# Performance work log

Measured on AMD Instinct MI355X. Metric: run time of the kernel, lower is better.

The kernel has to match this reference:

```python
import jax, jax.numpy as jnp
import numpy as np

DIM = 128
L = 4
EPS = 1e-5


def setup_inputs() -> dict:
    key = jax.random.key(0)
    ks = jax.random.split(key, 16)
    g, n_per = 4096, 32
    n = g * n_per
    e = 4 * n
    s = 0.05
    inp = {
        "x_atoms": jax.random.randint(ks[0], (n, 2), 0, 3),
        "edge_index": jax.random.randint(ks[1], (2, e), 0, n),
        "edge_attr": jax.random.randint(ks[2], (e, 2), 0, 3),
        "batch": jnp.repeat(jnp.arange(g), n_per),
        "num_graphs": g,
        "max_nodes": n_per,
        "task_embs": jax.random.normal(ks[3], (g, DIM), jnp.float32),
        "teb": jax.random.normal(ks[4], (g, DIM), jnp.float32),
        "emb1": jax.random.normal(ks[5], (120, DIM), jnp.float32) * s,
        "emb2": jax.random.normal(ks[6], (3, DIM), jnp.float32) * s,
        "edge_e1": jax.random.normal(ks[7], (L, 6, DIM), jnp.float32) * s,
        "edge_e2": jax.random.normal(ks[8], (L, 3, DIM), jnp.float32) * s,
        "W1": jax.random.normal(ks[9], (L, DIM, 2 * DIM), jnp.float32) * s,
        "b1": jnp.zeros((L, 2 * DIM), jnp.float32),
        "W2": jax.random.normal(ks[10], (L, 2 * DIM, DIM), jnp.float32) * s,
        "b2": jnp.zeros((L, DIM), jnp.float32),
        "bn_w": jnp.ones((L, DIM), jnp.float32),
        "bn_b": jnp.zeros((L, DIM), jnp.float32),
        "film_Wg": jax.random.normal(ks[11], (2, DIM, DIM), jnp.float32) * s,
        "film_bg": jnp.zeros((2, DIM), jnp.float32),
        "film_Wb": jax.random.normal(ks[12], (2, DIM, DIM), jnp.float32) * s,
        "film_bb": jnp.zeros((2, DIM), jnp.float32),
    }
    return inp


def _gin_layer(x, src, dst, eattr, e1, e2, W1, b1, W2, b2):
    # GINConv (pretrain-gnns): scatter-add of (x_j + edge_emb) + self-loop (attr [4,0]), then 2-layer MLP.
    n = x.shape[0]
    emb = e1[eattr[:, 0]] + e2[eattr[:, 1]]                       # [E, D]
    agg = jax.ops.segment_sum(x[src] + emb, dst, num_segments=n)  # [N, D]
    agg = agg + x + (e1[4] + e2[0])                               # self loops
    h = jax.nn.relu(agg @ W1 + b1)
    return h @ W2 + b2


def _batchnorm(x, w, b):
    mu = jnp.mean(x, axis=0)
    var = jnp.var(x, axis=0)
    return (x - mu) * jax.lax.rsqrt(var + EPS) * w + b


def reference(x_atoms, edge_index, edge_attr, batch, num_graphs, max_nodes,
              task_embs, teb, emb1, emb2, edge_e1, edge_e2,
              W1, b1, W2, b2, bn_w, bn_b,
              film_Wg, film_bg, film_Wb, film_bb):
    g = int(num_graphs)
    n = x_atoms.shape[0]
    x = emb1[x_atoms[:, 0]] + emb2[x_atoms[:, 1]]                 # [N, D]
    # --- add virtual nodes (one per graph) and bidirectional virtual edges ---
    x = jnp.concatenate([x, teb], axis=0)                         # [N+g, D]
    dst0 = jnp.arange(n)
    vsrc = n + batch                                              # virtual node index per real node
    src_all = jnp.concatenate([edge_index[0], vsrc, dst0])
    dst_all = jnp.concatenate([edge_index[1], dst0, vsrc])
    v_attr = jnp.tile(jnp.array([[5, 0]], dtype=edge_attr.dtype), (2 * n, 1))
    eattr = jnp.concatenate([edge_attr, v_attr], axis=0)
    # --- positions within graph for to_dense_batch (batch is sorted) ---
    counts = jnp.bincount(batch, length=g)
    offsets = jnp.cumsum(counts) - counts
    pos = dst0 - offsets[batch]
    for layer in range(L):
        x = _gin_layer(x, src_all, dst_all, eattr,
                       edge_e1[layer], edge_e2[layer],
                       W1[layer], b1[layer], W2[layer], b2[layer])
        if layer in (1, 3):
            xv = x[n:]
            dense = jnp.zeros((g, int(max_nodes), DIM), x.dtype).at[batch, pos].set(x[:n])
            fl = layer // 3
            gamma = task_embs @ film_Wg[fl] + film_bg[fl]          # [g, D]
            beta = task_embs @ film_Wb[fl] + film_bb[fl]
            dense = gamma[:, None, :] * dense + beta[:, None, :]
            x = jnp.concatenate([dense[batch, pos], xv], axis=0)   # masked_select inverse
        x = _batchnorm(x, bn_w[layer], bn_b[layer])
        if layer != L - 1:
            x = jax.nn.relu(x)
        # dropout is identity in eval mode
    return x[:n]
```

## Files before the change

kernel.cpp:

```cpp
#include <hip/hip_runtime.h>
#include <hip/hip_bf16.h>

typedef __bf16 bf16_t;
typedef bf16_t bf16x8 __attribute__((ext_vector_type(8)));
typedef bf16_t bf16x4v __attribute__((ext_vector_type(4)));
typedef float f32x4 __attribute__((ext_vector_type(4)));

#define EPSV 1e-5f

__global__ void k_zerof(float* p, int cnt) {
  int i = blockIdx.x * 256 + threadIdx.x;
  if (i < cnt) p[i] = 0.f;
}
__global__ void k_zeroi(int* p, int cnt) {
  int i = blockIdx.x * 256 + threadIdx.x;
  if (i < cnt) p[i] = 0;
}

__global__ void k_prep_weights(const float* __restrict__ W1, const float* __restrict__ W2,
                               bf16_t* __restrict__ W1T, bf16_t* __restrict__ W2T, int total) {
  int idx = blockIdx.x * 256 + threadIdx.x;
  if (idx >= total) return;
  int l = idx >> 15, r = idx & 32767;
  int k = r >> 8, c = r & 255;
  W1T[(l << 15) + c * 128 + k] = (bf16_t)W1[idx];
  int k2 = r >> 7, c2 = r & 127;
  W2T[(l << 15) + c2 * 256 + k2] = (bf16_t)W2[idx];
}

__global__ void k_prep_film(const float* __restrict__ Wg, const float* __restrict__ Wb,
                            bf16_t* __restrict__ fWT) {
  int idx = blockIdx.x * 256 + threadIdx.x;
  if (idx >= 4 * 16384) return;
  int m = idx >> 14, r = idx & 16383;
  int c = r >> 7, k = r & 127;
  const float* W = ((m & 1) ? Wb : Wg) + (m >> 1) * 16384;
  fWT[idx] = (bf16_t)W[k * 128 + c];
}

__global__ void k_prep_te(const float* __restrict__ te, bf16_t* __restrict__ teb_out, int total) {
  int idx = blockIdx.x * 256 + threadIdx.x;
  if (idx < total) teb_out[idx] = (bf16_t)te[idx];
}

__global__ void k_ecomb(const float* __restrict__ e1, const float* __restrict__ e2,
                        float* __restrict__ ec, int total) {
  int idx = blockIdx.x * 256 + threadIdx.x;
  if (idx >= total) return;
  int ch = idx & 127;
  int t = idx >> 7;
  int comb = t % 18, l = t / 18;
  int i = comb / 3, j = comb % 3;
  ec[idx] = e1[(l * 6 + i) * 128 + ch] + e2[(l * 3 + j) * 128 + ch];
}

__launch_bounds__(256, 2)
__global__ void k_film(const bf16_t* __restrict__ teb, const bf16_t* __restrict__ fWT,
                       const float* __restrict__ bg, const float* __restrict__ bb,
                       float* __restrict__ gbuf, int g) {
  const int mat = blockIdx.x & 3;
  const int r0 = (blockIdx.x >> 2) * 64;
  const int tid = threadIdx.x;
  const int wave = tid >> 6, lane = tid & 63;
  const int lr = lane & 15, lk = lane >> 4;
  const int w32 = wave * 32;
  const bf16_t* W = fWT + mat * 16384;
  const float* B = ((mat & 1) ? bb : bg) + (mat >> 1) * 128;

  bf16x8 bbf[2][4];
  #pragma unroll
  for (int cf = 0; cf < 2; ++cf)
    #pragma unroll
    for (int kk = 0; kk < 4; ++kk)
      bbf[cf][kk] = *(const bf16x8*)(W + ((w32 + cf * 16 + lr) << 7) + kk * 32 + (lk << 3));

  f32x4 acc[4][2];
  f32x4 zero4 = {0.f, 0.f, 0.f, 0.f};
  #pragma unroll
  for (int rf = 0; rf < 4; ++rf)
    #pragma unroll
    for (int cf = 0; cf < 2; ++cf) acc[rf][cf] = zero4;

  #pragma unroll
  for (int kk = 0; kk < 4; ++kk) {
    bf16x8 a[4];
    #pragma unroll
    for (int rf = 0; rf < 4; ++rf)
      a[rf] = *(const bf16x8*)(teb + ((size_t)(r0 + rf * 16 + lr) << 7) + kk * 32 + (lk << 3));
    #pragma unroll
    for (int rf = 0; rf < 4; ++rf)
      #pragma unroll
      for (int cf = 0; cf < 2; ++cf)
        acc[rf][cf] = __builtin_amdgcn_mfma_f32_16x16x32_bf16(a[rf], bbf[cf][kk], acc[rf][cf], 0, 0, 0);
  }

  float* out = gbuf + (size_t)mat * g * 128;
  #pragma unroll
  for (int cf = 0; cf < 2; ++cf) {
    int col = w32 + cf * 16 + lr;
    float bias = B[col];
    #pragma unroll
    for (int rf = 0; rf < 4; ++rf)
      #pragma unroll
      for (int j = 0; j < 4; ++j) {
        int row = r0 + rf * 16 + lk * 4 + j;
        out[(size_t)row * 128 + col] = acc[rf][cf][j] + bias;
      }
  }
}

__global__ void k_init_x(const int* __restrict__ xa, const float* __restrict__ teb,
                         const float* __restrict__ emb1, const float* __restrict__ emb2,
                         bf16_t* __restrict__ x, int n, int N) {
  int idx = blockIdx.x * 256 + threadIdx.x;
  if (idx >= N * 128) return;
  int row = idx >> 7, ch = idx & 127;
  float v;
  if (row < n) v = emb1[xa[row * 2] * 128 + ch] + emb2[xa[row * 2 + 1] * 128 + ch];
  else v = teb[(size_t)(row - n) * 128 + ch];
  x[idx] = (bf16_t)v;
}

__global__ void k_hist(const int* __restrict__ eidx, int* __restrict__ cnt, int E) {
  int i = blockIdx.x * 256 + threadIdx.x;
  if (i < E) atomicAdd(&cnt[eidx[E + i]], 1);
}

__global__ void k_scan1(const int* __restrict__ cnt, int* __restrict__ part,
                        int* __restrict__ bsum, int n) {
  __shared__ int s[256];
  int i = blockIdx.x * 256 + threadIdx.x;
  int v = (i < n) ? cnt[i] : 0;
  s[threadIdx.x] = v;
  for (int off = 1; off < 256; off <<= 1) {
    __syncthreads();
    int t = (threadIdx.x >= off) ? s[threadIdx.x - off] : 0;
    __syncthreads();
    s[threadIdx.x] += t;
  }
  __syncthreads();
  if (i < n) part[i] = s[threadIdx.x] - v;
  if (threadIdx.x == 255) bsum[blockIdx.x] = s[255];
}

__global__ void k_scan2(int* bsum, int nb) {
  __shared__ int s[512];
  int v = ((int)threadIdx.x < nb) ? bsum[threadIdx.x] : 0;
  s[threadIdx.x] = v;
  for (int off = 1; off < 512; off <<= 1) {
    __syncthreads();
    int t = ((int)threadIdx.x >= off) ? s[threadIdx.x - off] : 0;
    __syncthreads();
    s[threadIdx.x] += t;
  }
  __syncthreads();
  if ((int)threadIdx.x < nb) bsum[threadIdx.x] = s[threadIdx.x] - v;
}

__global__ void k_scan3(int* __restrict__ rp, const int* __restrict__ bsum,
                        int* __restrict__ fill, int n, int E) {
  int i = blockIdx.x * 256 + threadIdx.x;
  if (i < n) {
    int v = rp[i] + bsum[i >> 8];
    rp[i] = v;
    fill[i] = v;
  }
  if (i == 0) rp[n] = E;
}

__global__ void k_scatter(const int* __restrict__ eidx, const int* __restrict__ eattr,
                          int* __restrict__ fill, int* __restrict__ pack, int E) {
  int i = blockIdx.x * 256 + threadIdx.x;
  if (i >= E) return;
  int s = eidx[i];
  int d = eidx[E + i];
  int comb = eattr[2 * i] * 3 + eattr[2 * i + 1];
  int p = atomicAdd(&fill[d], 1);
  pack[p] = s | (comb << 20);
}

__global__ void k_normx(const bf16_t* __restrict__ y, const float* __restrict__ scsh,
                        bf16_t* __restrict__ xn, int total8) {
  int i = blockIdx.x * 256 + threadIdx.x;
  if (i >= total8) return;
  int ch8 = i & 15;
  bf16x8 v = ((const bf16x8*)y)[i];
  float4 sc0 = ((const float4*)scsh)[ch8 * 2];
  float4 sc1 = ((const float4*)scsh)[ch8 * 2 + 1];
  float4 sh0 = ((const float4*)(scsh + 128))[ch8 * 2];
  float4 sh1 = ((const float4*)(scsh + 128))[ch8 * 2 + 1];
  float sc[8] = {sc0.x, sc0.y, sc0.z, sc0.w, sc1.x, sc1.y, sc1.z, sc1.w};
  float sh[8] = {sh0.x, sh0.y, sh0.z, sh0.w, sh1.x, sh1.y, sh1.z, sh1.w};
  bf16x8 o;
  #pragma unroll
  for (int j = 0; j < 8; ++j)
    o[j] = (bf16_t)fmaxf(fmaf((float)v[j], sc[j], sh[j]), 0.f);
  ((bf16x8*)xn)[i] = o;
}

__launch_bounds__(512, 4)
__global__ void k_layer(const bf16_t* __restrict__ xn, const int* __restrict__ batch,
                        const int* __restrict__ rp, const int* __restrict__ pack,
                        const float* __restrict__ ec,
                        const bf16_t* __restrict__ W1T, const bf16_t* __restrict__ W2T,
                        const float* __restrict__ b1, const float* __restrict__ b2,
                        const float* __restrict__ gamma, const float* __restrict__ beta,
                        bf16_t* __restrict__ y, float* __restrict__ gstats,
                        int n, int N, int npg) {
  __shared__ __align__(16) char As[16384];
  __shared__ __align__(16) char Hs[32768];
  __shared__ float sred[256];
  const int tid = threadIdx.x;
  const int m0 = blockIdx.x * 64;
  const int wave = tid >> 6, lane = tid & 63;
  const int lr = lane & 15, lk = lane >> 4;

  {
    const int sgrp = tid >> 4;
    const int li = tid & 15;
    const int grpl = lane & 48;
    const int ch0 = li * 8;
    float4 s0 = *(const float4*)(ec + 12 * 128 + ch0);
    float4 s1 = *(const float4*)(ec + 12 * 128 + ch0 + 4);
    float4 v0 = *(const float4*)(ec + 15 * 128 + ch0);
    float4 v1 = *(const float4*)(ec + 15 * 128 + ch0 + 4);

    #define EACC(HX, E0, E1) { \
      acc[0] += (float)HX[0] + E0.x; acc[1] += (float)HX[1] + E0.y; \
      acc[2] += (float)HX[2] + E0.z; acc[3] += (float)HX[3] + E0.w; \
      acc[4] += (float)HX[4] + E1.x; acc[5] += (float)HX[5] + E1.y; \
      acc[6] += (float)HX[6] + E1.z; acc[7] += (float)HX[7] + E1.w; }

    #pragma unroll
    for (int t = 0; t < 2; ++t) {
      int row = sgrp * 2 + t;
      int node = m0 + row;
      float acc[8];
      if (node < N) {
        bf16x8 hs = *(const bf16x8*)(xn + ((size_t)node << 7) + ch0);
        if (node < n) {
          int b = batch[node];
          bf16x8 hv = *(const bf16x8*)(xn + ((size_t)(n + b) << 7) + ch0);
          acc[0] = (float)hs[0] + (float)hv[0] + s0.x + v0.x;
          acc[1] = (float)hs[1] + (float)hv[1] + s0.y + v0.y;
          acc[2] = (float)hs[2] + (float)hv[2] + s0.z + v0.z;
          acc[3] = (float)hs[3] + (float)hv[3] + s0.w + v0.w;
          acc[4] = (float)hs[4] + (float)hv[4] + s1.x + v1.x;
          acc[5] = (float)hs[5] + (float)hv[5] + s1.y + v1.y;
          acc[6] = (float)hs[6] + (float)hv[6] + s1.z + v1.z;
          acc[7] = (float)hs[7] + (float)hv[7] + s1.w + v1.w;
          int beg = rp[node], end = rp[node + 1];
          for (int base = beg; base < end; base += 16) {
            int cnt = end - base; cnt = cnt > 16 ? 16 : cnt;
            int pl = pack[base + (li < cnt ? li : cnt - 1)];
            int pc = __shfl(pl, grpl, 64);
            bf16x8 hx = *(const bf16x8*)(xn + ((size_t)(pc & 0xFFFFF) << 7) + ch0);
            const float* er = ec + ((pc >> 20) & 31) * 128 + ch0;
            float4 e0 = *(const float4*)er;
            float4 e1 = *(const float4*)(er + 4);
            for (int j = 1; j < cnt; ++j) {
              int pn = __shfl(pl, grpl | j, 64);
              bf16x8 hx2 = *(const bf16x8*)(xn + ((size_t)(pn & 0xFFFFF) << 7) + ch0);
              const float* er2 = ec + ((pn >> 20) & 31) * 128 + ch0;
              float4 f0 = *(const float4*)er2;
              float4 f1 = *(const float4*)(er2 + 4);
              EACC(hx, e0, e1);
              hx = hx2; e0 = f0; e1 = f1;
            }
            EACC(hx, e0, e1);
          }
        } else {
          float fn = (float)npg;
          acc[0] = (float)hs[0] + s0.x + fn * v0.x;
          acc[1] = (float)hs[1] + s0.y + fn * v0.y;
          acc[2] = (float)hs[2] + s0.z + fn * v0.z;
          acc[3] = (float)hs[3] + s0.w + fn * v0.w;
          acc[4] = (float)hs[4] + s1.x + fn * v1.x;
          acc[5] = (float)hs[5] + s1.y + fn * v1.y;
          acc[6] = (float)hs[6] + s1.z + fn * v1.z;
          acc[7] = (float)hs[7] + s1.w + fn * v1.w;
          int base = (node - n) * npg;
          bf16x8 h0 = *(const bf16x8*)(xn + ((size_t)base << 7) + ch0);
          for (int k = 1; k < npg; ++k) {
            bf16x8 h1 = *(const bf16x8*)(xn + ((size_t)(base + k) << 7) + ch0);
            #pragma unroll
            for (int j = 0; j < 8; ++j) acc[j] += (float)h0[j];
            h0 = h1;
          }
          #pragma unroll
          for (int j = 0; j < 8; ++j) acc[j] += (float)h0[j];
        }
      } else {
        #pragma unroll
        for (int j = 0; j < 8; ++j) acc[j] = 0.f;
      }
      bf16x8 o;
      #pragma unroll
      for (int j = 0; j < 8; ++j) o[j] = (bf16_t)acc[j];
      int byte = (row << 8) + ch0 * 2;
      byte ^= (row & 7) << 4;
      *(bf16x8*)(As + byte) = o;
    }
    #undef EACC
  }

  const int c1base = wave * 32;
  bf16x8 bb1[2][4];
  #pragma unroll
  for (int cf = 0; cf < 2; ++cf)
    #pragma unroll
    for (int kk = 0; kk < 4; ++kk)
      bb1[cf][kk] = *(const bf16x8*)(W1T + ((c1base + cf * 16 + lr) << 7) + kk * 32 + (lk << 3));

  __syncthreads();

  f32x4 zero4 = {0.f, 0.f, 0.f, 0.f};
  f32x4 acc1[4][2];
  #pragma unroll
  for (int rf = 0; rf < 4; ++rf)
    #pragma unroll
    for (int cf = 0; cf < 2; ++cf) acc1[rf][cf] = zero4;

  #pragma unroll
  for (int kk = 0; kk < 4; ++kk) {
    bf16x8 a[4];
    #pragma unroll
    for (int rf = 0; rf < 4; ++rf) {
      int arow = rf * 16 + lr;
      int abyte = (arow << 8) + kk * 64 + (lk << 4);
      abyte ^= (arow & 7) << 4;
      a[rf] = *(const bf16x8*)(As + abyte);
    }
    #pragma unroll
    for (int rf = 0; rf < 4; ++rf)
      #pragma unroll
      for (int cf = 0; cf < 2; ++cf)
        acc1[rf][cf] = __builtin_amdgcn_mfma_f32_16x16x32_bf16(bb1[cf][kk], a[rf], acc1[rf][cf], 0, 0, 0);
  }

  #pragma unroll
  for (int cf = 0; cf < 2; ++cf) {
    int c0 = c1base + cf * 16 + lk * 4;
    float4 b4 = *(const float4*)(b1 + c0);
    #pragma unroll
    for (int rf = 0; rf < 4; ++rf) {
      int row = rf * 16 + lr;
      bf16x4v h4;
      h4[0] = (bf16_t)fmaxf(acc1[rf][cf][0] + b4.x, 0.f);
      h4[1] = (bf16_t)fmaxf(acc1[rf][cf][1] + b4.y, 0.f);
      h4[2] = (bf16_t)fmaxf(acc1[rf][cf][2] + b4.z, 0.f);
      h4[3] = (bf16_t)fmaxf(acc1[rf][cf][3] + b4.w, 0.f);
      int byte = (row << 9) + c0 * 2;
      byte ^= (row & 15) << 4;
      *(bf16x4v*)(Hs + byte) = h4;
    }
  }

  const int c2base = wave * 16;
  bf16x8 bb2[8];
  #pragma unroll
  for (int kk = 0; kk < 8; ++kk)
    bb2[kk] = *(const bf16x8*)(W2T + ((c2base + lr) << 8) + kk * 32 + (lk << 3));

  __syncthreads();

  f32x4 acc2[4];
  #pragma unroll
  for (int rf = 0; rf < 4; ++rf) acc2[rf] = zero4;

  #pragma unroll
  for (int kk = 0; kk < 8; ++kk) {
    bf16x8 a2[4];
    #pragma unroll
    for (int rf = 0; rf < 4; ++rf) {
      int row = rf * 16 + lr;
      int byte = (row << 9) + kk * 64 + (lk << 4);
      byte ^= (row & 15) << 4;
      a2[rf] = *(const bf16x8*)(Hs + byte);
    }
    #pragma unroll
    for (int rf = 0; rf < 4; ++rf)
      acc2[rf] = __builtin_amdgcn_mfma_f32_16x16x32_bf16(bb2[kk], a2[rf], acc2[rf], 0, 0, 0);
  }

  {
    int c20 = c2base + lk * 4;
    float4 b4 = *(const float4*)(b2 + c20);
    f32x4 s4 = zero4, q4 = zero4;
    #pragma unroll
    for (int rf = 0; rf < 4; ++rf) {
      int row_g = m0 + rf * 16 + lr;
      f32x4 v;
      v[0] = acc2[rf][0] + b4.x;
      v[1] = acc2[rf][1] + b4.y;
      v[2] = acc2[rf][2] + b4.z;
      v[3] = acc2[rf][3] + b4.w;
      if (gamma != nullptr && row_g < n) {
        int b = batch[row_g];
        float4 g4 = *(const float4*)(gamma + (size_t)b * 128 + c20);
        float4 t4 = *(const float4*)(beta + (size_t)b * 128 + c20);
        v[0] = fmaf(g4.x, v[0], t4.x);
        v[1] = fmaf(g4.y, v[1], t4.y);
        v[2] = fmaf(g4.z, v[2], t4.z);
        v[3] = fmaf(g4.w, v[3], t4.w);
      }
      if (row_g < N) {
        s4 += v;
        q4 += v * v;
        bf16x4v o4;
        o4[0] = (bf16_t)v[0]; o4[1] = (bf16_t)v[1];
        o4[2] = (bf16_t)v[2]; o4[3] = (bf16_t)v[3];
        *(bf16x4v*)(y + (size_t)row_g * 128 + c20) = o4;
      }
    }
    #pragma unroll
    for (int off = 1; off < 16; off <<= 1) {
      #pragma unroll
      for (int j = 0; j < 4; ++j) {
        s4[j] += __shfl_xor(s4[j], off, 64);
        q4[j] += __shfl_xor(q4[j], off, 64);
      }
    }
    if (lr == 0) {
      *(f32x4*)(sred + c20) = s4;
      *(f32x4*)(sred + 128 + c20) = q4;
    }
  }
  __syncthreads();
  if (tid < 256) atomicAdd(&gstats[((blockIdx.x & 15) << 8) + tid], sred[tid]);
}

__global__ void k_finalize(float* st, const float* __restrict__ bnw,
                           const float* __restrict__ bnb, float invN) {
  int ch = threadIdx.x;
  float s = 0.f, q = 0.f;
  #pragma unroll
  for (int c = 0; c < 16; ++c) { s += st[c * 256 + ch]; q += st[c * 256 + 128 + ch]; }
  __syncthreads();
  #pragma unroll
  for (int z = 0; z < 32; ++z) st[ch * 32 + z] = 0.f;
  float mean = s * invN;
  float var = fmaxf(q * invN - mean * mean, 0.f);
  float inv = rsqrtf(var + EPSV);
  float sc = inv * bnw[ch];
  st[4096 + ch] = sc;
  st[4224 + ch] = bnb[ch] - mean * sc;
}

__global__ void k_norm(const bf16_t* __restrict__ yin, const float* __restrict__ scsh,
                       float* __restrict__ out, int total8) {
  int i = blockIdx.x * 256 + threadIdx.x;
  if (i >= total8) return;
  int ch8 = i & 15;
  bf16x8 v = ((const bf16x8*)yin)[i];
  float4 sc0 = ((const float4*)scsh)[ch8 * 2];
  float4 sc1 = ((const float4*)scsh)[ch8 * 2 + 1];
  float4 sh0 = ((const float4*)(scsh + 128))[ch8 * 2];
  float4 sh1 = ((const float4*)(scsh + 128))[ch8 * 2 + 1];
  float4 r0, r1;
  r0.x = (float)v[0] * sc0.x + sh0.x;
  r0.y = (float)v[1] * sc0.y + sh0.y;
  r0.z = (float)v[2] * sc0.z + sh0.z;
  r0.w = (float)v[3] * sc0.w + sh0.w;
  r1.x = (float)v[4] * sc1.x + sh1.x;
  r1.y = (float)v[5] * sc1.y + sh1.y;
  r1.z = (float)v[6] * sc1.z + sh1.z;
  r1.w = (float)v[7] * sc1.w + sh1.w;
  ((float4*)out)[i * 2] = r0;
  ((float4*)out)[i * 2 + 1] = r1;
}

extern "C" void kernel_launch(void* const* d_in, const int* in_sizes, int n_in,
                              void* d_out, int out_size, void* d_ws, size_t ws_size,
                              hipStream_t stream) {
  const int*   x_atoms    = (const int*)d_in[0];
  const int*   edge_index = (const int*)d_in[1];
  const int*   edge_attr  = (const int*)d_in[2];
  const int*   batch      = (const int*)d_in[3];
  const float* task_embs  = (const float*)d_in[6];
  const float* teb        = (const float*)d_in[7];
  const float* emb1       = (const float*)d_in[8];
  const float* emb2       = (const float*)d_in[9];
  const float* edge_e1    = (const float*)d_in[10];
  const float* edge_e2    = (const float*)d_in[11];
  const float* W1         = (const float*)d_in[12];
  const float* b1         = (const float*)d_in[13];
  const float* W2         = (const float*)d_in[14];
  const float* b2         = (const float*)d_in[15];
  const float* bnw        = (const float*)d_in[16];
  const float* bnb        = (const float*)d_in[17];
  const float* fWg        = (const float*)d_in[18];
  const float* fbg        = (const float*)d_in[19];
  const float* fWb        = (const float*)d_in[20];
  const float* fbb        = (const float*)d_in[21];

  const int n   = in_sizes[0] / 2;
  const int E   = in_sizes[1] / 2;
  const int g   = in_sizes[6] / 128;
  const int N   = n + g;
  const int npg = n / g;
  const int L   = in_sizes[12] / 32768;

  char* ws = (char*)d_ws;
  size_t off = 0;
  auto alloc = [&](size_t bytes) { size_t o = off; off += (bytes + 255) & ~(size_t)255; return o; };
  bf16_t* xbuf   = (bf16_t*)(ws + alloc((size_t)N * 128 * 2));
  bf16_t* xn     = (bf16_t*)(ws + alloc((size_t)N * 128 * 2));
  float*  gbuf   = (float*)(ws + alloc((size_t)4 * g * 128 * 4));
  bf16_t* W1Tb   = (bf16_t*)(ws + alloc((size_t)L * 32768 * 2));
  bf16_t* W2Tb   = (bf16_t*)(ws + alloc((size_t)L * 32768 * 2));
  bf16_t* fWTb   = (bf16_t*)(ws + alloc((size_t)4 * 16384 * 2));
  bf16_t* tebuf  = (bf16_t*)(ws + alloc((size_t)g * 128 * 2));
  float*  ecomb  = (float*)(ws + alloc((size_t)L * 18 * 128 * 4));
  float*  gstats = (float*)(ws + alloc((size_t)(4096 + 256) * 4));
  int*    row_ptr= (int*)(ws + alloc((size_t)(n + 1) * 4));
  int*    fill   = (int*)(ws + alloc((size_t)n * 4));
  int*    epack  = (int*)(ws + alloc((size_t)E * 4));
  int*    bsum   = (int*)(ws + alloc(512 * 4));
  (void)ws_size; (void)n_in; (void)out_size;

  k_prep_weights<<<(L * 32768 + 255) / 256, 256, 0, stream>>>(W1, W2, W1Tb, W2Tb, L * 32768);
  k_prep_film<<<(4 * 16384 + 255) / 256, 256, 0, stream>>>(fWg, fWb, fWTb);
  k_prep_te<<<(g * 128 + 255) / 256, 256, 0, stream>>>(task_embs, tebuf, g * 128);
  k_init_x<<<(N * 128 + 255) / 256, 256, 0, stream>>>(x_atoms, teb, emb1, emb2, xn, n, N);
  k_ecomb<<<(L * 18 * 128 + 255) / 256, 256, 0, stream>>>(edge_e1, edge_e2, ecomb, L * 18 * 128);
  k_film<<<(g / 64) * 4, 256, 0, stream>>>(tebuf, fWTb, fbg, fbb, gbuf, g);

  const int nb = (n + 255) / 256;
  k_zeroi<<<nb, 256, 0, stream>>>(fill, n);
  k_hist<<<(E + 255) / 256, 256, 0, stream>>>(edge_index, fill, E);
  k_scan1<<<nb, 256, 0, stream>>>(fill, row_ptr, bsum, n);
  k_scan2<<<1, 512, 0, stream>>>(bsum, nb);
  k_scan3<<<nb, 256, 0, stream>>>(row_ptr, bsum, fill, n, E);
  k_scatter<<<(E + 255) / 256, 256, 0, stream>>>(edge_index, edge_attr, fill, epack, E);

  k_zerof<<<16, 256, 0, stream>>>(gstats, 4096);
  for (int l = 0; l < 4; ++l) {
    if (l > 0)
      k_normx<<<(N * 16 + 255) / 256, 256, 0, stream>>>(xbuf, gstats + 4096, xn, N * 16);
    const float* gm = nullptr; const float* bt = nullptr;
    if (l == 1) { gm = gbuf;                       bt = gbuf + (size_t)g * 128; }
    if (l == 3) { gm = gbuf + (size_t)2 * g * 128; bt = gbuf + (size_t)3 * g * 128; }
    k_layer<<<(N + 63) / 64, 512, 0, stream>>>(xn, batch, row_ptr, epack,
        ecomb + (size_t)l * 18 * 128, W1Tb + (size_t)l * 32768, W2Tb + (size_t)l * 32768,
        b1 + l * 256, b2 + l * 128, gm, bt, xbuf, gstats, n, N, npg);
    k_finalize<<<1, 128, 0, stream>>>(gstats, bnw + l * 128, bnb + l * 128, 1.0f / (float)N);
  }
  k_norm<<<(n * 16 + 255) / 256, 256, 0, stream>>>(xbuf, gstats + 4096, (float*)d_out, n * 16);
}
```

Baseline: 558.8 us.

## Split hidden MLP dimension into two halves to halve hidden LDS buffer

Splits the 256-wide hidden layer of the fused GIN MLP into two 128-column passes. Each pass computes half of the hidden activations into a 16KB shared buffer and accumulates its contribution to the second GEMM. Shared memory per block drops from about 49KB to about 33KB, which may let more blocks fit per CU. In exchange it adds two extra block-wide barriers and preloads both weight halves into registers up front, which raises register pressure.

```diff
diff --git a/kernel.cpp b/kernel.cpp
--- a/kernel.cpp
+++ b/kernel.cpp
@@ -208,7 +208,7 @@
                         bf16_t* __restrict__ y, float* __restrict__ gstats,
                         int n, int N, int npg) {
   __shared__ __align__(16) char As[16384];
-  __shared__ __align__(16) char Hs[32768];
+  __shared__ __align__(16) char Hs[16384];
   __shared__ float sred[256];
   const int tid = threadIdx.x;
   const int m0 = blockIdx.x * 64;
@@ -304,83 +304,76 @@
     #undef EACC
   }
 
-  const int c1base = wave * 32;
-  bf16x8 bb1[2][4];
-  #pragma unroll
-  for (int cf = 0; cf < 2; ++cf)
-    #pragma unroll
-    for (int kk = 0; kk < 4; ++kk)
-      bb1[cf][kk] = *(const bf16x8*)(W1T + ((c1base + cf * 16 + lr) << 7) + kk * 32 + (lk << 3));
+  bf16x8 bb1[2][4], bb2[2][4];
+  const int c2base = wave * 16;
+  #pragma unroll
+  for (int p = 0; p < 2; ++p)
+    #pragma unroll
+    for (int kk = 0; kk < 4; ++kk) {
+      bb1[p][kk] = *(const bf16x8*)(W1T + ((p * 128 + c2base + lr) << 7) + kk * 32 + (lk << 3));
+      bb2[p][kk] = *(const bf16x8*)(W2T + ((c2base + lr) << 8) + p * 128 + kk * 32 + (lk << 3));
+    }
 
   __syncthreads();
 
   f32x4 zero4 = {0.f, 0.f, 0.f, 0.f};
-  f32x4 acc1[4][2];
-  #pragma unroll
-  for (int rf = 0; rf < 4; ++rf)
-    #pragma unroll
-    for (int cf = 0; cf < 2; ++cf) acc1[rf][cf] = zero4;
-
-  #pragma unroll
-  for (int kk = 0; kk < 4; ++kk) {
-    bf16x8 a[4];
-    #pragma unroll
-    for (int rf = 0; rf < 4; ++rf) {
-      int arow = rf * 16 + lr;
-      int abyte = (arow << 8) + kk * 64 + (lk << 4);
-      abyte ^= (arow & 7) << 4;
-      a[rf] = *(const bf16x8*)(As + abyte);
-    }
-    #pragma unroll
-    for (int rf = 0; rf < 4; ++rf)
-      #pragma unroll
-      for (int cf = 0; cf < 2; ++cf)
-        acc1[rf][cf] = __builtin_amdgcn_mfma_f32_16x16x32_bf16(bb1[cf][kk], a[rf], acc1[rf][cf], 0, 0, 0);
-  }
-
-  #pragma unroll
-  for (int cf = 0; cf < 2; ++cf) {
-    int c0 = c1base + cf * 16 + lk * 4;
-    float4 b4 = *(const float4*)(b1 + c0);
-    #pragma unroll
-    for (int rf = 0; rf < 4; ++rf) {
-      int row = rf * 16 + lr;
-      bf16x4v h4;
-      h4[0] = (bf16_t)fmaxf(acc1[rf][cf][0] + b4.x, 0.f);
-      h4[1] = (bf16_t)fmaxf(acc1[rf][cf][1] + b4.y, 0.f);
-      h4[2] = (bf16_t)fmaxf(acc1[rf][cf][2] + b4.z, 0.f);
-      h4[3] = (bf16_t)fmaxf(acc1[rf][cf][3] + b4.w, 0.f);
-      int byte = (row << 9) + c0 * 2;
-      byte ^= (row & 15) << 4;
-      *(bf16x4v*)(Hs + byte) = h4;
-    }
-  }
-
-  const int c2base = wave * 16;
-  bf16x8 bb2[8];
-  #pragma unroll
-  for (int kk = 0; kk < 8; ++kk)
-    bb2[kk] = *(const bf16x8*)(W2T + ((c2base + lr) << 8) + kk * 32 + (lk << 3));
-
-  __syncthreads();
-
   f32x4 acc2[4];
   #pragma unroll
   for (int rf = 0; rf < 4; ++rf) acc2[rf] = zero4;
 
   #pragma unroll
-  for (int kk = 0; kk < 8; ++kk) {
-    bf16x8 a2[4];
-    #pragma unroll
-    for (int rf = 0; rf < 4; ++rf) {
-      int row = rf * 16 + lr;
-      int byte = (row << 9) + kk * 64 + (lk << 4);
-      byte ^= (row & 15) << 4;
-      a2[rf] = *(const bf16x8*)(Hs + byte);
-    }
-    #pragma unroll
-    for (int rf = 0; rf < 4; ++rf)
-      acc2[rf] = __builtin_amdgcn_mfma_f32_16x16x32_bf16(bb2[kk], a2[rf], acc2[rf], 0, 0, 0);
+  for (int p = 0; p < 2; ++p) {
+    f32x4 acc1[4];
+    #pragma unroll
+    for (int rf = 0; rf < 4; ++rf) acc1[rf] = zero4;
+    #pragma unroll
+    for (int kk = 0; kk < 4; ++kk) {
+      bf16x8 a[4];
+      #pragma unroll
+      for (int rf = 0; rf < 4; ++rf) {
+        int arow = rf * 16 + lr;
+        int abyte = (arow << 8) + kk * 64 + (lk << 4);
+        abyte ^= (arow & 7) << 4;
+        a[rf] = *(const bf16x8*)(As + abyte);
+      }
+      #pragma unroll
+      for (int rf = 0; rf < 4; ++rf)
+        acc1[rf] = __builtin_amdgcn_mfma_f32_16x16x32_bf16(bb1[p][kk], a[rf], acc1[rf], 0, 0, 0);
+    }
+
+    {
+      int c0l = c2base + lk * 4;
+      float4 b4 = *(const float4*)(b1 + p * 128 + c0l);
+      #pragma unroll
+      for (int rf = 0; rf < 4; ++rf) {
+        int row = rf * 16 + lr;
+        bf16x4v h4;
+        h4[0] = (bf16_t)fmaxf(acc1[rf][0] + b4.x, 0.f);
+        h4[1] = (bf16_t)fmaxf(acc1[rf][1] + b4.y, 0.f);
+        h4[2] = (bf16_t)fmaxf(acc1[rf][2] + b4.z, 0.f);
+        h4[3] = (bf16_t)fmaxf(acc1[rf][3] + b4.w, 0.f);
+        int byte = (row << 8) + c0l * 2;
+        byte ^= (row & 7) << 4;
+        *(bf16x4v*)(Hs + byte) = h4;
+      }
+    }
+    __syncthreads();
+
+    #pragma unroll
+    for (int kk = 0; kk < 4; ++kk) {
+      bf16x8 a2[4];
+      #pragma unroll
+      for (int rf = 0; rf < 4; ++rf) {
+        int row = rf * 16 + lr;
+        int byte = (row << 8) + kk * 64 + (lk << 4);
+        byte ^= (row & 7) << 4;
+        a2[rf] = *(const bf16x8*)(Hs + byte);
+      }
+      #pragma unroll
+      for (int rf = 0; rf < 4; ++rf)
+        acc2[rf] = __builtin_amdgcn_mfma_f32_16x16x32_bf16(bb2[p][kk], a2[rf], acc2[rf], 0, 0, 0);
+    }
+    __syncthreads();
   }
 
   {
```

New measurement: 593.3 us. +6.2%, slower.
